# Optimization experiments

Measured on AMD Instinct MI355X. Metric: run time of the kernel, lower is better.

Reference implementation:

```python
import jax, jax.numpy as jnp
import numpy as np

N_NODES = 100000
N_EDGES = 3200000
IN_DIM = 128
HIDDEN = 128
N_GRAPHS = 64


def setup_inputs() -> dict:
    key = jax.random.key(0)
    ks = jax.random.split(key, 16)
    feat = jax.random.normal(ks[0], (N_NODES, IN_DIM), dtype=jnp.float32)
    src = jax.random.randint(ks[1], (N_EDGES,), 0, N_NODES, dtype=jnp.int32)
    dst = jax.random.randint(ks[2], (N_EDGES,), 0, N_NODES, dtype=jnp.int32)
    graph_ids = jnp.sort(jax.random.randint(ks[3], (N_NODES,), 0, N_GRAPHS, dtype=jnp.int32))
    # GraphConv weights (in_feats, out_feats) + bias, DGL default glorot-ish scale
    def lin(k, fi, fo):
        s = 1.0 / np.sqrt(fi)
        kw, kb = jax.random.split(k)
        W = jax.random.uniform(kw, (fi, fo), jnp.float32, -s, s)
        b = jax.random.uniform(kb, (fo,), jnp.float32, -s, s)
        return W, b
    W1, b1 = lin(ks[4], IN_DIM, HIDDEN)
    W2, b2 = lin(ks[5], HIDDEN, HIDDEN)
    # MLPReadout(128, 1, L=3): 128->64->32->16->1
    Wm0, bm0 = lin(ks[6], 128, 64)
    Wm1, bm1 = lin(ks[7], 64, 32)
    Wm2, bm2 = lin(ks[8], 32, 16)
    Wm3, bm3 = lin(ks[9], 16, 1)
    return dict(feat=feat, src=src, dst=dst, graph_ids=graph_ids, num_graphs=N_GRAPHS,
                W1=W1, b1=b1, W2=W2, b2=b2,
                Wm0=Wm0, bm0=bm0, Wm1=Wm1, bm1=bm1, Wm2=Wm2, bm2=bm2, Wm3=Wm3, bm3=bm3)


def reference(feat, src, dst, graph_ids, num_graphs,
              W1, b1, W2, b2,
              Wm0, bm0, Wm1, bm1, Wm2, bm2, Wm3, bm3):
    N = feat.shape[0]
    ones_e = jnp.ones(src.shape[0], dtype=feat.dtype)
    # DGL GraphConv norm='both': D_out^{-1/2} on src side, D_in^{-1/2} on dst side,
    # degrees clamped to >=1 (allow_zero_in_degree=True)
    deg_out = jnp.clip(jax.ops.segment_sum(ones_e, src, num_segments=N), 1.0)
    deg_in = jnp.clip(jax.ops.segment_sum(ones_e, dst, num_segments=N), 1.0)
    norm_src = jax.lax.rsqrt(deg_out)[:, None]  # [N,1]
    norm_dst = jax.lax.rsqrt(deg_in)[:, None]

    def gconv(h, W, b):
        h = h * norm_src
        agg = jax.ops.segment_sum(h[src], dst, num_segments=N)  # SpMM: [N,d]
        return agg * norm_dst @ W + b

    h = jax.nn.relu(gconv(feat, W1, b1))
    h = jax.nn.relu(gconv(h, W2, b2))

    # dgl.mean_nodes: per-graph mean over nodes
    counts = jnp.clip(jax.ops.segment_sum(jnp.ones(N, dtype=h.dtype), graph_ids, num_segments=num_graphs), 1.0)
    hg = jax.ops.segment_sum(h, graph_ids, num_segments=num_graphs) / counts[:, None]  # [G, hidden]

    # MLPReadout
    y = jax.nn.relu(hg @ Wm0 + bm0)
    y = jax.nn.relu(y @ Wm1 + bm1)
    y = jax.nn.relu(y @ Wm2 + bm2)
    return y @ Wm3 + bm3  # [G, 1]
```

## Files before the change

### kernel.cpp

```cpp
#include <hip/hip_runtime.h>
#include <hip/hip_fp16.h>

#define N_NODES 100000
#define N_EDGES 3200000
#define DIM 128
#define NG 64
#define GS_CHUNKS 16

#define KSH 9
#define BKT 512
#define NBKT ((N_NODES + BKT - 1) / BKT)
#define CHUNK 8192
#define NBLK ((N_EDGES + CHUNK - 1) / CHUNK)

using f16x8 = __attribute__((ext_vector_type(8))) _Float16;
using f32x4 = __attribute__((ext_vector_type(4))) float;

__global__ __launch_bounds__(256) void k_hist1(const int* __restrict__ src, const int* __restrict__ dst,
                                               int* __restrict__ histD, int* __restrict__ histS,
                                               int* __restrict__ rowtot) {
    __shared__ int hD[4 * NBKT];
    __shared__ int hS[4 * NBKT];
    int t = threadIdx.x, blk = blockIdx.x;
    int w = t >> 6;
    for (int i = t; i < 4 * NBKT; i += 256) { hD[i] = 0; hS[i] = 0; }
    __syncthreads();
    int base = blk * CHUNK;
    for (int i = t; i < CHUNK; i += 256) {
        int e = base + i;
        if (e < N_EDGES) {
            atomicAdd(&hD[w * NBKT + (dst[e] >> KSH)], 1);
            atomicAdd(&hS[w * NBKT + (src[e] >> KSH)], 1);
        }
    }
    __syncthreads();
    for (int i = t; i < NBKT; i += 256) {
        int d = hD[i] + hD[NBKT + i] + hD[2 * NBKT + i] + hD[3 * NBKT + i];
        int s = hS[i] + hS[NBKT + i] + hS[2 * NBKT + i] + hS[3 * NBKT + i];
        histD[i * NBLK + blk] = d;
        histS[i * NBLK + blk] = s;
        atomicAdd(&rowtot[i], d);
        atomicAdd(&rowtot[NBKT + i], s);
    }
}

__global__ __launch_bounds__(512) void k_rowapply(int* __restrict__ histD, int* __restrict__ histS,
                                                  const int* __restrict__ rowtot) {
    __shared__ int sh[512];
    __shared__ int red[256];
    int r = blockIdx.x;
    int half = (r < NBKT) ? 0 : 1;
    int pos = half ? (r - NBKT) : r;
    int* a = half ? (histS + (size_t)pos * NBLK) : (histD + (size_t)pos * NBLK);
    int t = threadIdx.x;
    if (t < 256) red[t] = (t < pos) ? rowtot[half * NBKT + t] : 0;
    __syncthreads();
    for (int off = 128; off > 0; off >>= 1) {
        if (t < off) red[t] += red[t + off];
        __syncthreads();
    }
    int basev = red[0];
    int x = (t < NBLK) ? a[t] : 0;
    sh[t] = x; __syncthreads();
    for (int off = 1; off < 512; off <<= 1) {
        int y = sh[t]; int u = (t >= off) ? sh[t - off] : 0;
        __syncthreads(); sh[t] = y + u; __syncthreads();
    }
    if (t < NBLK) a[t] = sh[t] - x + basev;
}

__global__ __launch_bounds__(256) void k_scatter1(const int* __restrict__ src, const int* __restrict__ dst,
                                                  const int* __restrict__ histD, const int* __restrict__ histS,
                                                  int* __restrict__ bufD, unsigned short* __restrict__ bufS) {
    __shared__ int cD[NBKT];
    __shared__ int cS[NBKT];
    int t = threadIdx.x, blk = blockIdx.x;
    for (int i = t; i < NBKT; i += 256) {
        cD[i] = histD[i * NBLK + blk];
        cS[i] = histS[i * NBLK + blk];
    }
    __syncthreads();
    int base = blk * CHUNK;
    for (int i = t; i < CHUNK; i += 256) {
        int e = base + i;
        if (e < N_EDGES) {
            int s = src[e], d = dst[e];
            int pD = atomicAdd(&cD[d >> KSH], 1);
            bufD[pD] = ((d & (BKT - 1)) << 17) | s;
            int pS = atomicAdd(&cS[s >> KSH], 1);
            bufS[pS] = (unsigned short)(s & (BKT - 1));
        }
    }
}

__global__ __launch_bounds__(256) void k_pass2s(const unsigned short* __restrict__ bufS,
                                                const int* __restrict__ histS,
                                                float* __restrict__ norm_src) {
    __shared__ int binc[BKT];
    int b = blockIdx.x, t = threadIdx.x;
    int start = histS[b * NBLK];
    int end = (b + 1 < NBKT) ? histS[(b + 1) * NBLK] : N_EDGES;
    for (int i = t; i < BKT; i += 256) binc[i] = 0;
    __syncthreads();
    for (int i = start + t; i < end; i += 256) atomicAdd(&binc[bufS[i]], 1);
    __syncthreads();
    int nb = N_NODES - b * BKT; if (nb > BKT) nb = BKT;
    for (int j = t; j < nb; j += 256) {
        int c = binc[j]; if (c < 1) c = 1;
        norm_src[b * BKT + j] = rsqrtf((float)c);
    }
}

__global__ __launch_bounds__(256) void k_pass2(const int* __restrict__ bufD,
                                               const int* __restrict__ histD,
                                               int* __restrict__ rowptr, float* __restrict__ norm_dst,
                                               int* __restrict__ col) {
    __shared__ int binc[BKT];
    __shared__ int binoff[BKT];
    int b = blockIdx.x, t = threadIdx.x;
    int start = histD[b * NBLK];
    int end = (b + 1 < NBKT) ? histD[(b + 1) * NBLK] : N_EDGES;
    for (int i = t; i < BKT; i += 256) binc[i] = 0;
    __syncthreads();
    for (int i = start + t; i < end; i += 256) atomicAdd(&binc[bufD[i] >> 17], 1);
    __syncthreads();
    if (t < 64) {
        int base8 = t * 8;
        int loc[8]; int s8 = 0;
        #pragma unroll
        for (int k = 0; k < 8; k++) { loc[k] = s8; s8 += binc[base8 + k]; }
        int x = s8;
        #pragma unroll
        for (int off = 1; off < 64; off <<= 1) {
            int y = __shfl_up(x, off);
            if (t >= off) x += y;
        }
        int excl = x - s8;
        #pragma unroll
        for (int k = 0; k < 8; k++) binoff[base8 + k] = excl + loc[k];
    }
    __syncthreads();
    int nb = N_NODES - b * BKT; if (nb > BKT) nb = BKT;
    for (int j = t; j < nb; j += 256) {
        rowptr[b * BKT + j] = start + binoff[j];
        int c = binc[j]; if (c < 1) c = 1;
        norm_dst[b * BKT + j] = rsqrtf((float)c);
    }
    if (b == NBKT - 1 && t == 0) rowptr[N_NODES] = N_EDGES;
    __syncthreads();
    for (int i = t; i < BKT; i += 256) binc[i] = binoff[i];
    __syncthreads();
    for (int i = start + t; i < end; i += 256) {
        int v = bufD[i];
        int ld = v >> 17, s = v & 0x1FFFF;
        int p = atomicAdd(&binc[ld], 1);
        col[start + p] = s;
    }
}

__global__ __launch_bounds__(256) void k_cast8(const float* __restrict__ in,
                                               const float* __restrict__ norm_src,
                                               unsigned* __restrict__ out) {
    int i4 = blockIdx.x * 256 + threadIdx.x;
    const int TOT = N_NODES * DIM / 4;
    if (i4 >= TOT) return;
    int row = i4 >> 5;
    float sc = norm_src[row];
    float4 v = ((const float4*)in)[i4];
    unsigned w = 0;
    w = __builtin_amdgcn_cvt_pk_fp8_f32(v.x * sc, v.y * sc, w, 0);
    w = __builtin_amdgcn_cvt_pk_fp8_f32(v.z * sc, v.w * sc, w, 1);
    out[i4] = w;
}

#define ACC8(r) do {                                                                  \
    auto p0 = __builtin_amdgcn_cvt_pk_f32_fp8((r).x, 0); a0 += p0[0]; a1 += p0[1];    \
    auto p1 = __builtin_amdgcn_cvt_pk_f32_fp8((r).x, 1); a2 += p1[0]; a3 += p1[1];    \
    auto p2 = __builtin_amdgcn_cvt_pk_f32_fp8((r).y, 0); a4 += p2[0]; a5 += p2[1];    \
    auto p3 = __builtin_amdgcn_cvt_pk_f32_fp8((r).y, 1); a6 += p3[0]; a7 += p3[1];    \
    auto p4 = __builtin_amdgcn_cvt_pk_f32_fp8((r).z, 0); a8 += p4[0]; a9 += p4[1];    \
    auto p5 = __builtin_amdgcn_cvt_pk_f32_fp8((r).z, 1); a10 += p5[0]; a11 += p5[1];  \
    auto p6 = __builtin_amdgcn_cvt_pk_f32_fp8((r).w, 0); a12 += p6[0]; a13 += p6[1];  \
    auto p7 = __builtin_amdgcn_cvt_pk_f32_fp8((r).w, 1); a14 += p7[0]; a15 += p7[1];  \
} while (0)

__global__ __launch_bounds__(256) void k_spmm8(const unsigned char* __restrict__ in,
                       const int* __restrict__ rowptr, const int* __restrict__ col,
                       const float* __restrict__ norm_dst, __half2* __restrict__ out) {
    int wid = (blockIdx.x * 256 + threadIdx.x) >> 6;
    int lane = threadIdx.x & 63;
    int rg = lane >> 3, l8 = lane & 7;
    int node = wid * 8 + rg;
    if (node >= N_NODES) return;
    int jb = rowptr[node], je = rowptr[node + 1];
    float a0 = 0.f, a1 = 0.f, a2 = 0.f, a3 = 0.f, a4 = 0.f, a5 = 0.f, a6 = 0.f, a7 = 0.f;
    float a8 = 0.f, a9 = 0.f, a10 = 0.f, a11 = 0.f, a12 = 0.f, a13 = 0.f, a14 = 0.f, a15 = 0.f;
    int j = jb;
    for (; j + 2 <= je; j += 2) {
        int s0 = col[j], s1 = col[j + 1];
        uint4 r0 = *(const uint4*)&in[(size_t)s0 * 128 + l8 * 16];
        uint4 r1 = *(const uint4*)&in[(size_t)s1 * 128 + l8 * 16];
        ACC8(r0);
        ACC8(r1);
    }
    if (j < je) {
        int s0 = col[j];
        uint4 r0 = *(const uint4*)&in[(size_t)s0 * 128 + l8 * 16];
        ACC8(r0);
    }
    float nd = norm_dst[node];
    __half2 h0 = __floats2half2_rn(a0 * nd, a1 * nd);
    __half2 h1 = __floats2half2_rn(a2 * nd, a3 * nd);
    __half2 h2 = __floats2half2_rn(a4 * nd, a5 * nd);
    __half2 h3 = __floats2half2_rn(a6 * nd, a7 * nd);
    __half2 h4 = __floats2half2_rn(a8 * nd, a9 * nd);
    __half2 h5 = __floats2half2_rn(a10 * nd, a11 * nd);
    __half2 h6 = __floats2half2_rn(a12 * nd, a13 * nd);
    __half2 h7 = __floats2half2_rn(a14 * nd, a15 * nd);
    uint4 o0, o1;
    o0.x = *(unsigned*)&h0; o0.y = *(unsigned*)&h1;
    o0.z = *(unsigned*)&h2; o0.w = *(unsigned*)&h3;
    o1.x = *(unsigned*)&h4; o1.y = *(unsigned*)&h5;
    o1.z = *(unsigned*)&h6; o1.w = *(unsigned*)&h7;
    *(uint4*)&out[(size_t)node * 64 + l8 * 8] = o0;
    *(uint4*)&out[(size_t)node * 64 + l8 * 8 + 4] = o1;
}

template <bool SCALE, bool OUT8>
__global__ __launch_bounds__(256) void k_gemm_mfma(const __half* __restrict__ A,
        const float* __restrict__ W, const float* __restrict__ bias,
        const float* __restrict__ rowscale, void* __restrict__ outp) {
    __shared__ _Float16 lds[128 * 136];
    int tid = threadIdx.x;
    for (int idx = tid * 4; idx < DIM * DIM; idx += 256 * 4) {
        int k = idx >> 7, n = idx & 127;
        float4 w = *(const float4*)&W[idx];
        lds[(n + 0) * 136 + k] = (_Float16)w.x;
        lds[(n + 1) * 136 + k] = (_Float16)w.y;
        lds[(n + 2) * 136 + k] = (_Float16)w.z;
        lds[(n + 3) * 136 + k] = (_Float16)w.w;
    }
    __syncthreads();
    int wv = tid >> 6, lane = tid & 63;
    int rbase = blockIdx.x * 64 + wv * 16;
    int l15 = lane & 15, kg = lane >> 4;
    int arow = rbase + l15; if (arow >= N_NODES) arow = N_NODES - 1;
    const _Float16* Af = (const _Float16*)A + (size_t)arow * DIM + kg * 8;
    f16x8 a0 = *(const f16x8*)(Af + 0);
    f16x8 a1 = *(const f16x8*)(Af + 32);
    f16x8 a2 = *(const f16x8*)(Af + 64);
    f16x8 a3 = *(const f16x8*)(Af + 96);
    f32x4 acc[8];
    #pragma unroll
    for (int nt = 0; nt < 8; nt++) acc[nt] = (f32x4){0.f, 0.f, 0.f, 0.f};
    #pragma unroll
    for (int nt = 0; nt < 8; nt++) {
        const _Float16* bb = &lds[(nt * 16 + l15) * 136 + kg * 8];
        f16x8 b0 = *(const f16x8*)(bb + 0);
        f16x8 b1 = *(const f16x8*)(bb + 32);
        f16x8 b2 = *(const f16x8*)(bb + 64);
        f16x8 b3 = *(const f16x8*)(bb + 96);
        acc[nt] = __builtin_amdgcn_mfma_f32_16x16x32_f16(a0, b0, acc[nt], 0, 0, 0);
        acc[nt] = __builtin_amdgcn_mfma_f32_16x16x32_f16(a1, b1, acc[nt], 0, 0, 0);
        acc[nt] = __builtin_amdgcn_mfma_f32_16x16x32_f16(a2, b2, acc[nt], 0, 0, 0);
        acc[nt] = __builtin_amdgcn_mfma_f32_16x16x32_f16(a3, b3, acc[nt], 0, 0, 0);
    }
    __syncthreads();
    float bsc[4];
    #pragma unroll
    for (int r = 0; r < 4; r++) {
        if (SCALE) {
            int row = rbase + kg * 4 + r; if (row >= N_NODES) row = N_NODES - 1;
            bsc[r] = rowscale[row];
        } else bsc[r] = 1.f;
    }
    #pragma unroll
    for (int nt = 0; nt < 8; nt++) {
        float bv = bias[nt * 16 + l15];
        #pragma unroll
        for (int r = 0; r < 4; r++) {
            float v = fmaxf(acc[nt][r] + bv, 0.f) * bsc[r];
            lds[(size_t)(wv * 16 + kg * 4 + r) * 136 + nt * 16 + l15] = (_Float16)v;
        }
    }
    __syncthreads();
    #pragma unroll
    for (int t = 0; t < 4; t++) {
        int lrow = wv * 16 + t * 4 + kg;
        int grow = rbase + t * 4 + kg;
        f16x8 v = *(const f16x8*)&lds[(size_t)lrow * 136 + l15 * 8];
        if (grow < N_NODES) {
            if (OUT8) {
                unsigned w0 = 0, w1 = 0;
                w0 = __builtin_amdgcn_cvt_pk_fp8_f32((float)v[0], (float)v[1], w0, 0);
                w0 = __builtin_amdgcn_cvt_pk_fp8_f32((float)v[2], (float)v[3], w0, 1);
                w1 = __builtin_amdgcn_cvt_pk_fp8_f32((float)v[4], (float)v[5], w1, 0);
                w1 = __builtin_amdgcn_cvt_pk_fp8_f32((float)v[6], (float)v[7], w1, 1);
                uint2 o; o.x = w0; o.y = w1;
                *(uint2*)&((unsigned char*)outp)[(size_t)grow * 128 + l15 * 8] = o;
            } else {
                *(f16x8*)&((_Float16*)outp)[(size_t)grow * DIM + l15 * 8] = v;
            }
        }
    }
}

__global__ __launch_bounds__(256) void k_graphsum_part(const __half2* __restrict__ h,
                           const int* __restrict__ gids, float* __restrict__ partial) {
    __shared__ float redx[256];
    __shared__ float redy[256];
    __shared__ int sb[2];
    int g = blockIdx.x;
    int c = blockIdx.y;
    if (threadIdx.x == 0) {
        int lo = 0, hi = N_NODES;
        while (lo < hi) { int mid = (lo + hi) >> 1; if (gids[mid] < g) lo = mid + 1; else hi = mid; }
        sb[0] = lo;
        lo = 0; hi = N_NODES;
        while (lo < hi) { int mid = (lo + hi) >> 1; if (gids[mid] <= g) lo = mid + 1; else hi = mid; }
        sb[1] = lo;
    }
    __syncthreads();
    int s = sb[0], e = sb[1];
    int p = threadIdx.x & 63;
    int r = threadIdx.x >> 6;
    int clen = (e - s + GS_CHUNKS - 1) / GS_CHUNKS;
    int b0 = s + c * clen;
    int b1 = b0 + clen; if (b1 > e) b1 = e;
    float ax = 0.f, ay = 0.f;
    for (int nd = b0 + r; nd < b1; nd += 4) {
        float2 f = __half22float2(h[(size_t)nd * 64 + p]);
        ax += f.x; ay += f.y;
    }
    redx[threadIdx.x] = ax; redy[threadIdx.x] = ay;
    __syncthreads();
    if (threadIdx.x < 64) {
        float sx = redx[threadIdx.x] + redx[threadIdx.x + 64] + redx[threadIdx.x + 128] + redx[threadIdx.x + 192];
        float sy = redy[threadIdx.x] + redy[threadIdx.x + 64] + redy[threadIdx.x + 128] + redy[threadIdx.x + 192];
        float* pp = &partial[((size_t)g * GS_CHUNKS + c) * DIM];
        pp[2 * threadIdx.x] = sx;
        pp[2 * threadIdx.x + 1] = sy;
    }
}

__global__ __launch_bounds__(128) void k_mlp(const float* __restrict__ partial,
                      const int* __restrict__ gids,
                      const float* __restrict__ Wm0, const float* __restrict__ bm0,
                      const float* __restrict__ Wm1, const float* __restrict__ bm1,
                      const float* __restrict__ Wm2, const float* __restrict__ bm2,
                      const float* __restrict__ Wm3, const float* __restrict__ bm3,
                      float* __restrict__ out) {
    __shared__ float hb[DIM];
    __shared__ float l0[64];
    __shared__ float l1[32];
    __shared__ float l2[16];
    __shared__ int scnt;
    int g = blockIdx.x;
    int t = threadIdx.x;
    if (t == 0) {
        int lo = 0, hi = N_NODES;
        while (lo < hi) { int mid = (lo + hi) >> 1; if (gids[mid] < g) lo = mid + 1; else hi = mid; }
        int s = lo;
        lo = 0; hi = N_NODES;
        while (lo < hi) { int mid = (lo + hi) >> 1; if (gids[mid] <= g) lo = mid + 1; else hi = mid; }
        int c = lo - s; if (c < 1) c = 1;
        scnt = c;
    }
    __syncthreads();
    float acc = 0.f;
    #pragma unroll
    for (int c = 0; c < GS_CHUNKS; c++)
        acc += partial[((size_t)g * GS_CHUNKS + c) * DIM + t];
    hb[t] = acc / (float)scnt;
    __syncthreads();
    if (t < 64) {
        float a = bm0[t];
        for (int k = 0; k < 128; k++) a += hb[k] * Wm0[k * 64 + t];
        l0[t] = fmaxf(a, 0.f);
    }
    __syncthreads();
    if (t < 32) {
        float a = bm1[t];
        for (int k = 0; k < 64; k++) a += l0[k] * Wm1[k * 32 + t];
        l1[t] = fmaxf(a, 0.f);
    }
    __syncthreads();
    if (t < 16) {
        float a = bm2[t];
        for (int k = 0; k < 32; k++) a += l1[k] * Wm2[k * 16 + t];
        l2[t] = fmaxf(a, 0.f);
    }
    __syncthreads();
    if (t == 0) {
        float a = bm3[0];
        for (int k = 0; k < 16; k++) a += l2[k] * Wm3[k];
        out[g] = a;
    }
}

extern "C" void kernel_launch(void* const* d_in, const int* in_sizes, int n_in,
                              void* d_out, int out_size, void* d_ws, size_t ws_size,
                              hipStream_t stream) {
    const float* feat = (const float*)d_in[0];
    const int*   src  = (const int*)d_in[1];
    const int*   dst  = (const int*)d_in[2];
    const int*   gids = (const int*)d_in[3];
    const float* W1   = (const float*)d_in[5];
    const float* b1   = (const float*)d_in[6];
    const float* W2   = (const float*)d_in[7];
    const float* b2   = (const float*)d_in[8];
    const float* Wm0  = (const float*)d_in[9];
    const float* bm0  = (const float*)d_in[10];
    const float* Wm1  = (const float*)d_in[11];
    const float* bm1  = (const float*)d_in[12];
    const float* Wm2  = (const float*)d_in[13];
    const float* bm2  = (const float*)d_in[14];
    const float* Wm3  = (const float*)d_in[15];
    const float* bm3  = (const float*)d_in[16];
    float* out = (float*)d_out;

    char* ws = (char*)d_ws;
    size_t off = 0;
    auto alloc = [&](size_t bytes) -> void* {
        void* p = ws + off;
        off += (bytes + 511) & ~(size_t)511;
        return p;
    };
    float* norm_src = (float*)alloc((size_t)N_NODES * 4);
    float* norm_dst = (float*)alloc((size_t)N_NODES * 4);
    int* rowptr   = (int*)alloc((size_t)(N_NODES + 1) * 4);
    int* histD    = (int*)alloc((size_t)NBKT * NBLK * 4);
    int* histS    = (int*)alloc((size_t)NBKT * NBLK * 4);
    int* rowtot   = (int*)alloc((size_t)(2 * NBKT) * 4);
    int* bufD     = (int*)alloc((size_t)N_EDGES * 4);
    int* colbuf   = (int*)alloc((size_t)N_EDGES * 4);
    unsigned char* feat8 = (unsigned char*)alloc((size_t)N_NODES * DIM);
    unsigned char* h8    = (unsigned char*)alloc((size_t)N_NODES * DIM);
    __half* s16   = (__half*)alloc((size_t)N_NODES * DIM * 2);
    __half* g16   = (__half*)alloc((size_t)N_NODES * DIM * 2);
    float* partial = (float*)alloc((size_t)NG * GS_CHUNKS * DIM * 4);
    unsigned short* bufS = (unsigned short*)colbuf;
    int* col = colbuf;

    hipMemsetAsync(rowtot, 0, (size_t)(2 * NBKT) * 4, stream);

    k_hist1<<<NBLK, 256, 0, stream>>>(src, dst, histD, histS, rowtot);
    k_rowapply<<<2 * NBKT, 512, 0, stream>>>(histD, histS, rowtot);
    k_scatter1<<<NBLK, 256, 0, stream>>>(src, dst, histD, histS, bufD, bufS);
    k_pass2s<<<NBKT, 256, 0, stream>>>(bufS, histS, norm_src);
    k_pass2<<<NBKT, 256, 0, stream>>>(bufD, histD, rowptr, norm_dst, col);

    k_cast8<<<(N_NODES * DIM / 4 + 255) / 256, 256, 0, stream>>>(feat, norm_src, (unsigned*)feat8);

    int sb2 = (N_NODES + 31) / 32;
    int gb = (N_NODES + 63) / 64;
    k_spmm8<<<sb2, 256, 0, stream>>>(feat8, rowptr, col, norm_dst, (__half2*)s16);
    k_gemm_mfma<true, true><<<gb, 256, 0, stream>>>(s16, W1, b1, norm_src, h8);
    k_spmm8<<<sb2, 256, 0, stream>>>(h8, rowptr, col, norm_dst, (__half2*)s16);
    k_gemm_mfma<false, false><<<gb, 256, 0, stream>>>(s16, W2, b2, nullptr, g16);

    dim3 gsg(NG, GS_CHUNKS);
    k_graphsum_part<<<gsg, 256, 0, stream>>>((const __half2*)g16, gids, partial);
    k_mlp<<<NG, 128, 0, stream>>>(partial, gids, Wm0, bm0, Wm1, bm1, Wm2, bm2, Wm3, bm3, out);
}
```

Before: 362.1 us.

## Split fp8 features into 32-column slabs and run SpMM per slab

Features are stored as four column slabs of 32 bytes per node, and each SpMM runs as four passes, one per slab, so each pass's gathered table (about 3.2 MB) fits better in cache. Within a pass, each 8-lane group splits into two halves that handle alternate edges, and the halves are combined with a shuffle. This trades four times the col-index reads and kernel launches, plus smaller 8-byte gathers, for better cache hit rates on the random gathers.

```diff
diff --git a/kernel.cpp b/kernel.cpp
--- a/kernel.cpp
+++ b/kernel.cpp
@@ -12,6 +12,8 @@
 #define NBKT ((N_NODES + BKT - 1) / BKT)
 #define CHUNK 8192
 #define NBLK ((N_EDGES + CHUNK - 1) / CHUNK)
+
+#define SLAB ((size_t)N_NODES * 32)
 
 using f16x8 = __attribute__((ext_vector_type(8))) _Float16;
 using f32x4 = __attribute__((ext_vector_type(4))) float;
@@ -160,70 +162,77 @@
 
 __global__ __launch_bounds__(256) void k_cast8(const float* __restrict__ in,
                                                const float* __restrict__ norm_src,
-                                               unsigned* __restrict__ out) {
+                                               unsigned char* __restrict__ slab) {
     int i4 = blockIdx.x * 256 + threadIdx.x;
     const int TOT = N_NODES * DIM / 4;
     if (i4 >= TOT) return;
     int row = i4 >> 5;
+    int f = (i4 & 31) * 4;
+    int slice = f >> 5;
+    int o = f & 31;
     float sc = norm_src[row];
     float4 v = ((const float4*)in)[i4];
     unsigned w = 0;
     w = __builtin_amdgcn_cvt_pk_fp8_f32(v.x * sc, v.y * sc, w, 0);
     w = __builtin_amdgcn_cvt_pk_fp8_f32(v.z * sc, v.w * sc, w, 1);
-    out[i4] = w;
-}
-
-#define ACC8(r) do {                                                                  \
+    *(unsigned*)&slab[(size_t)slice * SLAB + (size_t)row * 32 + o] = w;
+}
+
+#define ACCU2(r) do {                                                                 \
     auto p0 = __builtin_amdgcn_cvt_pk_f32_fp8((r).x, 0); a0 += p0[0]; a1 += p0[1];    \
     auto p1 = __builtin_amdgcn_cvt_pk_f32_fp8((r).x, 1); a2 += p1[0]; a3 += p1[1];    \
     auto p2 = __builtin_amdgcn_cvt_pk_f32_fp8((r).y, 0); a4 += p2[0]; a5 += p2[1];    \
     auto p3 = __builtin_amdgcn_cvt_pk_f32_fp8((r).y, 1); a6 += p3[0]; a7 += p3[1];    \
-    auto p4 = __builtin_amdgcn_cvt_pk_f32_fp8((r).z, 0); a8 += p4[0]; a9 += p4[1];    \
-    auto p5 = __builtin_amdgcn_cvt_pk_f32_fp8((r).z, 1); a10 += p5[0]; a11 += p5[1];  \
-    auto p6 = __builtin_amdgcn_cvt_pk_f32_fp8((r).w, 0); a12 += p6[0]; a13 += p6[1];  \
-    auto p7 = __builtin_amdgcn_cvt_pk_f32_fp8((r).w, 1); a14 += p7[0]; a15 += p7[1];  \
 } while (0)
 
-__global__ __launch_bounds__(256) void k_spmm8(const unsigned char* __restrict__ in,
+__global__ __launch_bounds__(256) void k_spmm8s(const unsigned char* __restrict__ slab,
                        const int* __restrict__ rowptr, const int* __restrict__ col,
-                       const float* __restrict__ norm_dst, __half2* __restrict__ out) {
+                       const float* __restrict__ norm_dst, __half2* __restrict__ out, int slice) {
     int wid = (blockIdx.x * 256 + threadIdx.x) >> 6;
     int lane = threadIdx.x & 63;
     int rg = lane >> 3, l8 = lane & 7;
     int node = wid * 8 + rg;
     if (node >= N_NODES) return;
+    int sub = l8 >> 2, q = l8 & 3;
     int jb = rowptr[node], je = rowptr[node + 1];
     float a0 = 0.f, a1 = 0.f, a2 = 0.f, a3 = 0.f, a4 = 0.f, a5 = 0.f, a6 = 0.f, a7 = 0.f;
-    float a8 = 0.f, a9 = 0.f, a10 = 0.f, a11 = 0.f, a12 = 0.f, a13 = 0.f, a14 = 0.f, a15 = 0.f;
     int j = jb;
-    for (; j + 2 <= je; j += 2) {
-        int s0 = col[j], s1 = col[j + 1];
-        uint4 r0 = *(const uint4*)&in[(size_t)s0 * 128 + l8 * 16];
-        uint4 r1 = *(const uint4*)&in[(size_t)s1 * 128 + l8 * 16];
-        ACC8(r0);
-        ACC8(r1);
+    for (; j + 4 <= je; j += 4) {
+        int s0 = col[j + sub];
+        int s1 = col[j + 2 + sub];
+        uint2 r0 = *(const uint2*)&slab[(size_t)s0 * 32 + q * 8];
+        uint2 r1 = *(const uint2*)&slab[(size_t)s1 * 32 + q * 8];
+        ACCU2(r0);
+        ACCU2(r1);
+    }
+    if (j + 2 <= je) {
+        int s0 = col[j + sub];
+        uint2 r0 = *(const uint2*)&slab[(size_t)s0 * 32 + q * 8];
+        ACCU2(r0);
+        j += 2;
     }
     if (j < je) {
-        int s0 = col[j];
-        uint4 r0 = *(const uint4*)&in[(size_t)s0 * 128 + l8 * 16];
-        ACC8(r0);
-    }
-    float nd = norm_dst[node];
-    __half2 h0 = __floats2half2_rn(a0 * nd, a1 * nd);
-    __half2 h1 = __floats2half2_rn(a2 * nd, a3 * nd);
-    __half2 h2 = __floats2half2_rn(a4 * nd, a5 * nd);
-    __half2 h3 = __floats2half2_rn(a6 * nd, a7 * nd);
-    __half2 h4 = __floats2half2_rn(a8 * nd, a9 * nd);
-    __half2 h5 = __floats2half2_rn(a10 * nd, a11 * nd);
-    __half2 h6 = __floats2half2_rn(a12 * nd, a13 * nd);
-    __half2 h7 = __floats2half2_rn(a14 * nd, a15 * nd);
-    uint4 o0, o1;
-    o0.x = *(unsigned*)&h0; o0.y = *(unsigned*)&h1;
-    o0.z = *(unsigned*)&h2; o0.w = *(unsigned*)&h3;
-    o1.x = *(unsigned*)&h4; o1.y = *(unsigned*)&h5;
-    o1.z = *(unsigned*)&h6; o1.w = *(unsigned*)&h7;
-    *(uint4*)&out[(size_t)node * 64 + l8 * 8] = o0;
-    *(uint4*)&out[(size_t)node * 64 + l8 * 8 + 4] = o1;
+        if (sub == 0) {
+            int s0 = col[j];
+            uint2 r0 = *(const uint2*)&slab[(size_t)s0 * 32 + q * 8];
+            ACCU2(r0);
+        }
+    }
+    a0 += __shfl_xor(a0, 4); a1 += __shfl_xor(a1, 4);
+    a2 += __shfl_xor(a2, 4); a3 += __shfl_xor(a3, 4);
+    a4 += __shfl_xor(a4, 4); a5 += __shfl_xor(a5, 4);
+    a6 += __shfl_xor(a6, 4); a7 += __shfl_xor(a7, 4);
+    if (sub == 0) {
+        float nd = norm_dst[node];
+        __half2 h0 = __floats2half2_rn(a0 * nd, a1 * nd);
+        __half2 h1 = __floats2half2_rn(a2 * nd, a3 * nd);
+        __half2 h2 = __floats2half2_rn(a4 * nd, a5 * nd);
+        __half2 h3 = __floats2half2_rn(a6 * nd, a7 * nd);
+        uint4 o;
+        o.x = *(unsigned*)&h0; o.y = *(unsigned*)&h1;
+        o.z = *(unsigned*)&h2; o.w = *(unsigned*)&h3;
+        *(uint4*)&out[(size_t)node * 64 + slice * 16 + q * 4] = o;
+    }
 }
 
 template <bool SCALE, bool OUT8>
@@ -296,8 +305,11 @@
                 w0 = __builtin_amdgcn_cvt_pk_fp8_f32((float)v[2], (float)v[3], w0, 1);
                 w1 = __builtin_amdgcn_cvt_pk_fp8_f32((float)v[4], (float)v[5], w1, 0);
                 w1 = __builtin_amdgcn_cvt_pk_fp8_f32((float)v[6], (float)v[7], w1, 1);
-                uint2 o; o.x = w0; o.y = w1;
-                *(uint2*)&((unsigned char*)outp)[(size_t)grow * 128 + l15 * 8] = o;
+                int f = l15 * 8;
+                int slice = f >> 5;
+                int o = f & 31;
+                uint2 ov; ov.x = w0; ov.y = w1;
+                *(uint2*)&((unsigned char*)outp)[(size_t)slice * SLAB + (size_t)grow * 32 + o] = ov;
             } else {
                 *(f16x8*)&((_Float16*)outp)[(size_t)grow * DIM + l15 * 8] = v;
             }
@@ -450,13 +462,15 @@
     k_pass2s<<<NBKT, 256, 0, stream>>>(bufS, histS, norm_src);
     k_pass2<<<NBKT, 256, 0, stream>>>(bufD, histD, rowptr, norm_dst, col);
 
-    k_cast8<<<(N_NODES * DIM / 4 + 255) / 256, 256, 0, stream>>>(feat, norm_src, (unsigned*)feat8);
+    k_cast8<<<(N_NODES * DIM / 4 + 255) / 256, 256, 0, stream>>>(feat, norm_src, feat8);
 
     int sb2 = (N_NODES + 31) / 32;
     int gb = (N_NODES + 63) / 64;
-    k_spmm8<<<sb2, 256, 0, stream>>>(feat8, rowptr, col, norm_dst, (__half2*)s16);
+    for (int s = 0; s < 4; ++s)
+        k_spmm8s<<<sb2, 256, 0, stream>>>(feat8 + (size_t)s * SLAB, rowptr, col, norm_dst, (__half2*)s16, s);
     k_gemm_mfma<true, true><<<gb, 256, 0, stream>>>(s16, W1, b1, norm_src, h8);
-    k_spmm8<<<sb2, 256, 0, stream>>>(h8, rowptr, col, norm_dst, (__half2*)s16);
+    for (int s = 0; s < 4; ++s)
+        k_spmm8s<<<sb2, 256, 0, stream>>>(h8 + (size_t)s * SLAB, rowptr, col, norm_dst, (__half2*)s16, s);
     k_gemm_mfma<false, false><<<gb, 256, 0, stream>>>(s16, W2, b2, nullptr, g16);
 
     dim3 gsg(NG, GS_CHUNKS);
```

Measured after the change: 475.1 us. 1.31x slower.
